# Kernel optimization log

Measured on AMD Instinct MI355X. Metric: run time of the kernel, lower is better.

Reference implementation:

```python
import jax, jax.numpy as jnp
import numpy as np

DIM = 1024
HEADS = 16
DIM_HEAD = 64
INNER = HEADS * DIM_HEAD
SCALE = DIM_HEAD ** -0.5


def setup_inputs() -> dict:
    key = jax.random.key(0)
    ks = jax.random.split(key, 9)
    B, N = 4, 4096
    x = jax.random.normal(ks[0], (B, N, DIM), dtype=jnp.float32)
    mask = jnp.ones((B, N), dtype=bool)
    s = 0.02
    W_qkv = jax.random.normal(ks[1], (DIM, INNER * 3), dtype=jnp.float32) * s
    w_q = jax.random.normal(ks[2], (DIM_HEAD,), dtype=jnp.float32) * s
    w_k = jax.random.normal(ks[3], (DIM_HEAD,), dtype=jnp.float32) * s
    W_r = jax.random.normal(ks[4], (DIM_HEAD, DIM_HEAD), dtype=jnp.float32) * s
    b_r = jnp.zeros((DIM_HEAD,), dtype=jnp.float32)
    W_out = jax.random.normal(ks[5], (INNER, DIM), dtype=jnp.float32) * s
    b_out = jnp.zeros((DIM,), dtype=jnp.float32)
    return {"x": x, "mask": mask, "W_qkv": W_qkv, "w_q": w_q, "w_k": w_k,
            "W_r": W_r, "b_r": b_r, "W_out": W_out, "b_out": b_out}


def reference(x, mask, W_qkv, w_q, w_k, W_r, b_r, W_out, b_out):
    B, N, D = x.shape
    h, dh = HEADS, DIM_HEAD
    mask_value = -jnp.finfo(x.dtype).max

    qkv = x @ W_qkv                                  # [B,N,3*inner]
    q, k, v = jnp.split(qkv, 3, axis=-1)
    tohead = lambda t: t.reshape(B, N, h, dh).transpose(0, 2, 1, 3)  # b h n d
    q, k, v = tohead(q), tohead(k), tohead(v)
    m = mask[:, None, :]                             # b 1 n

    # global query via softmax-pooled per-token logits
    q_logits = jnp.einsum('bhnd,d->bhn', q, w_q) * SCALE
    q_attn = jax.nn.softmax(jnp.where(m, q_logits, mask_value), axis=-1)
    global_q = jnp.einsum('bhn,bhnd->bhd', q_attn, q)[:, :, None, :]  # b h 1 d

    k = k * global_q
    k_logits = jnp.einsum('bhnd,d->bhn', k, w_k) * SCALE
    k_attn = jax.nn.softmax(jnp.where(m, k_logits, mask_value), axis=-1)
    global_k = jnp.einsum('bhn,bhnd->bhd', k_attn, k)[:, :, None, :]  # b h 1 d

    v = v * global_k
    r = jnp.einsum('bhnd,de->bhne', v, W_r) + b_r + q  # to_r(v) + q
    r = r.transpose(0, 2, 1, 3).reshape(B, N, h * dh)  # b n (h d)
    return r @ W_out + b_out
```

## Files before the change

### kernel.cpp

```cpp
#include <hip/hip_runtime.h>
#include <hip/hip_bf16.h>
#include <math.h>

#define B_    4
#define N_    4096
#define D_    1024
#define H_    16
#define DH_   64
#define M_TOT (B_ * N_)
#define QKV3  (3 * D_)
#define SCALE_ 0.125f
#define NSPLIT 4

typedef float f32x4 __attribute__((ext_vector_type(4)));
typedef __bf16 bf16x8 __attribute__((ext_vector_type(8)));
typedef unsigned short u16;
typedef unsigned int u32;

__device__ __forceinline__ float bf2f(u16 u) {
    union { u32 i; float f; } v; v.i = ((u32)u) << 16; return v.f;
}
__device__ __forceinline__ u16 f2bf(float f) {
    union { float f; u32 i; } v; v.f = f;
    u32 r = (v.i + 0x7fffu + ((v.i >> 16) & 1u)) >> 16;
    return (u16)r;
}

__global__ __launch_bounds__(256) void cvt_x(const float* __restrict__ in,
                                             u16* __restrict__ out, int n4) {
    int i = blockIdx.x * blockDim.x + threadIdx.x;
    if (i >= n4) return;
    float4 v = ((const float4*)in)[i];
    ushort4 o;
    o.x = f2bf(v.x); o.y = f2bf(v.y); o.z = f2bf(v.z); o.w = f2bf(v.w);
    ((ushort4*)out)[i] = o;
}

__global__ __launch_bounds__(256) void tcvt(const float* __restrict__ in,
                                            u16* __restrict__ out, int K, int N) {
    __shared__ float t[32][33];
    int n0 = blockIdx.x * 32, k0 = blockIdx.y * 32;
    int tx = threadIdx.x & 31, ty = threadIdx.x >> 5;
#pragma unroll
    for (int r = 0; r < 32; r += 8)
        t[ty + r][tx] = in[(size_t)(k0 + ty + r) * N + n0 + tx];
    __syncthreads();
#pragma unroll
    for (int r = 0; r < 32; r += 8)
        out[(size_t)(n0 + ty + r) * K + k0 + tx] = f2bf(t[tx][ty + r]);
}

#define BM 128
#define BN 128
#define BK 32

template <bool OUT_BF16, bool SCATTER>
__global__ __launch_bounds__(256) void gemm_bt(const u16* __restrict__ A,
                                               const u16* __restrict__ Bt,
                                               void* __restrict__ Cout,
                                               const float* __restrict__ bias,
                                               int M, int N, int K) {
    __shared__ u16 As[BM * BK];
    __shared__ u16 Bs[BN * BK];
    const int tid = threadIdx.x;
    const int wave = tid >> 6, lane = tid & 63;
    const int m0 = blockIdx.y * BM, n0 = blockIdx.x * BN;
    const int wr = wave & 1, wc = wave >> 1;

    f32x4 acc[4][4] = {};

    const int srow = lane >> 2;
    const int sk = (lane & 3) * 8;
    const u16* Ag = A + (size_t)(m0 + wave * 32 + srow) * K + sk;
    const u16* Bg = Bt + (size_t)(n0 + wave * 32 + srow) * K + sk;
    u16* Asw = &As[(wave * 32) * BK];
    u16* Bsw = &Bs[(wave * 32) * BK];

    const int fr = lane & 15;
    const int fk = (lane >> 4) * 8;

    for (int k0 = 0; k0 < K; k0 += BK) {
        __syncthreads();
        __builtin_amdgcn_global_load_lds(
            (__attribute__((address_space(1))) const void*)(Ag + k0),
            (__attribute__((address_space(3))) void*)Asw, 16, 0, 0);
        __builtin_amdgcn_global_load_lds(
            (__attribute__((address_space(1))) const void*)(Ag + k0 + 16 * K),
            (__attribute__((address_space(3))) void*)(Asw + 16 * BK), 16, 0, 0);
        __builtin_amdgcn_global_load_lds(
            (__attribute__((address_space(1))) const void*)(Bg + k0),
            (__attribute__((address_space(3))) void*)Bsw, 16, 0, 0);
        __builtin_amdgcn_global_load_lds(
            (__attribute__((address_space(1))) const void*)(Bg + k0 + 16 * K),
            (__attribute__((address_space(3))) void*)(Bsw + 16 * BK), 16, 0, 0);
        __syncthreads();

        bf16x8 af[4], bf[4];
#pragma unroll
        for (int i = 0; i < 4; i++)
            af[i] = *(const bf16x8*)&As[(wr * 64 + i * 16 + fr) * BK + fk];
#pragma unroll
        for (int i = 0; i < 4; i++)
            bf[i] = *(const bf16x8*)&Bs[(wc * 64 + i * 16 + fr) * BK + fk];
#pragma unroll
        for (int i = 0; i < 4; i++)
#pragma unroll
            for (int j = 0; j < 4; j++)
                acc[i][j] = __builtin_amdgcn_mfma_f32_16x16x32_bf16(af[i], bf[j], acc[i][j], 0, 0, 0);
    }

    const int cr = (lane >> 4) * 4;
    const int cc = lane & 15;
#pragma unroll
    for (int i = 0; i < 4; i++) {
#pragma unroll
        for (int j = 0; j < 4; j++) {
            const int row0 = m0 + wr * 64 + i * 16 + cr;
            const int col = n0 + wc * 64 + j * 16 + cc;
            const float bv = (!SCATTER && bias) ? bias[col] : 0.f;
#pragma unroll
            for (int r = 0; r < 4; r++) {
                const float v = acc[i][j][r] + bv;
                if (SCATTER) {
                    const int part = col >> 10, hh = (col >> 6) & (H_ - 1), e = col & (DH_ - 1);
                    const int row = row0 + r;
                    const int b = row >> 12, nn = row & (N_ - 1);
                    ((u16*)Cout)[(((size_t)(part * B_ + b) * H_ + hh) * N_ + nn) * DH_ + e] = f2bf(v);
                } else if (OUT_BF16) {
                    ((u16*)Cout)[(size_t)(row0 + r) * N + col] = f2bf(v);
                } else {
                    ((float*)Cout)[(size_t)(row0 + r) * N + col] = v;
                }
            }
        }
    }
}

template <bool KPHASE>
__global__ __launch_bounds__(256) void pool_partial(const u16* __restrict__ plane,
                                                    const float* __restrict__ wvec,
                                                    const float* __restrict__ gq_all,
                                                    float* __restrict__ part) {
    __shared__ float sm[32], sl[32], sacc[32][64];
    const int bh = blockIdx.x, s = blockIdx.y;
    const int tid = threadIdx.x;
    const int sub = tid >> 3, j = tid & 7;
    const size_t base = (size_t)bh * N_ * DH_ + (size_t)s * (N_ / NSPLIT) * DH_ + j * 8;

    float wv[8], gq[8];
#pragma unroll
    for (int i = 0; i < 8; i++) wv[i] = wvec[j * 8 + i];
    if (KPHASE) {
#pragma unroll
        for (int i = 0; i < 8; i++) gq[i] = gq_all[bh * 64 + j * 8 + i];
    }

    float m = -INFINITY, l = 0.f, acc[8];
#pragma unroll
    for (int i = 0; i < 8; i++) acc[i] = 0.f;
    for (int it = 0; it < N_ / NSPLIT / 32; it++) {
        const uint4 raw = *(const uint4*)(plane + base + (size_t)(it * 32 + sub) * DH_);
        const u16* pu = (const u16*)&raw;
        float f[8], p = 0.f;
#pragma unroll
        for (int i = 0; i < 8; i++) {
            f[i] = bf2f(pu[i]);
            if (KPHASE) f[i] *= gq[i];
            p += f[i] * wv[i];
        }
        p += __shfl_xor(p, 1); p += __shfl_xor(p, 2); p += __shfl_xor(p, 4);
        p *= SCALE_;
        const float mn = fmaxf(m, p);
        const float sc = __expf(m - mn);
        const float w = __expf(p - mn);
        m = mn; l = l * sc + w;
#pragma unroll
        for (int i = 0; i < 8; i++) acc[i] = acc[i] * sc + w * f[i];
    }
    if (j == 0) { sm[sub] = m; sl[sub] = l; }
#pragma unroll
    for (int i = 0; i < 8; i++) sacc[sub][j * 8 + i] = acc[i];
    __syncthreads();
    if (tid < 64) {
        float M = -INFINITY;
        for (int g = 0; g < 32; g++) M = fmaxf(M, sm[g]);
        float L = 0.f, ssum = 0.f;
        for (int g = 0; g < 32; g++) {
            const float e = __expf(sm[g] - M);
            L += sl[g] * e;
            ssum += sacc[g][tid] * e;
        }
        float* o = part + ((size_t)bh * NSPLIT + s) * 66;
        if (tid == 0) { o[0] = M; o[1] = L; }
        o[2 + tid] = ssum;
    }
}

__global__ __launch_bounds__(64) void pool_reduce(const float* __restrict__ part,
                                                  float* __restrict__ gout) {
    const int bh = blockIdx.x, e = threadIdx.x;
    float M = -INFINITY;
    for (int s = 0; s < NSPLIT; s++) M = fmaxf(M, part[((size_t)bh * NSPLIT + s) * 66]);
    float L = 0.f, ssum = 0.f;
    for (int s = 0; s < NSPLIT; s++) {
        const float* o = part + ((size_t)bh * NSPLIT + s) * 66;
        const float w = __expf(o[0] - M);
        L += o[1] * w;
        ssum += o[2 + e] * w;
    }
    gout[bh * 64 + e] = ssum / L;
}

__global__ __launch_bounds__(256) void apply_r_mfma(const u16* __restrict__ qkv,
                                                    const float* __restrict__ Wr,
                                                    const float* __restrict__ br,
                                                    const float* __restrict__ gk,
                                                    u16* __restrict__ rout) {
    __shared__ u16 Mt[64][136];
    const int bh = blockIdx.y;
    const int b = bh >> 4, h = bh & 15;
    const int tid = threadIdx.x, lane = tid & 63, wave = tid >> 6;

    for (int idx = tid; idx < 4096; idx += 256) {
        const int d = idx >> 6, e = idx & 63;
        Mt[e][d] = f2bf(gk[bh * 64 + d] * Wr[idx]);
        Mt[e][64 + d] = (d == e) ? (u16)0x3F80 : (u16)0;
    }
    __syncthreads();

    const size_t qbase = (size_t)bh * N_ * DH_;
    const size_t vbase = (size_t)(2 * B_ * H_ + bh) * N_ * DH_;
    const int row0 = blockIdx.x * 256 + wave * 64;
    const int fr = lane & 15;
    const int fk8 = (lane >> 4) * 8;
    f32x4 acc[4][4] = {};

#pragma unroll
    for (int ks = 0; ks < 4; ks++) {
        const int kd = ks * 32 + fk8;
        bf16x8 af[4], bf[4];
#pragma unroll
        for (int i = 0; i < 4; i++) {
            const int row = row0 + i * 16 + fr;
            const size_t off = (kd < 64) ? (vbase + (size_t)row * DH_ + kd)
                                         : (qbase + (size_t)row * DH_ + (kd - 64));
            af[i] = *(const bf16x8*)(qkv + off);
        }
#pragma unroll
        for (int j = 0; j < 4; j++)
            bf[j] = *(const bf16x8*)&Mt[j * 16 + fr][kd];
#pragma unroll
        for (int i = 0; i < 4; i++)
#pragma unroll
            for (int j = 0; j < 4; j++)
                acc[i][j] = __builtin_amdgcn_mfma_f32_16x16x32_bf16(af[i], bf[j], acc[i][j], 0, 0, 0);
    }

    const int cr = (lane >> 4) * 4;
    const int cc = lane & 15;
#pragma unroll
    for (int j = 0; j < 4; j++) {
        const int col = j * 16 + cc;
        const float bv = br[col];
#pragma unroll
        for (int i = 0; i < 4; i++) {
            const int row = row0 + i * 16 + cr;
#pragma unroll
            for (int r = 0; r < 4; r++)
                rout[(size_t)(b * N_ + row + r) * D_ + h * DH_ + col] = f2bf(acc[i][j][r] + bv);
        }
    }
}

extern "C" void kernel_launch(void* const* d_in, const int* in_sizes, int n_in,
                              void* d_out, int out_size, void* d_ws, size_t ws_size,
                              hipStream_t stream) {
    const float* x = (const float*)d_in[0];
    const float* W_qkv = (const float*)d_in[2];
    const float* w_q = (const float*)d_in[3];
    const float* w_k = (const float*)d_in[4];
    const float* W_r = (const float*)d_in[5];
    const float* b_r = (const float*)d_in[6];
    const float* W_out = (const float*)d_in[7];
    const float* b_out = (const float*)d_in[8];
    float* out = (float*)d_out;

    u16* xb = (u16*)d_ws;
    u16* wqkv = xb + (size_t)M_TOT * D_;
    u16* wout = wqkv + (size_t)QKV3 * D_;
    u16* qkv = wout + (size_t)D_ * D_;
    u16* rbuf = qkv + (size_t)M_TOT * QKV3;
    float* gq = (float*)(rbuf + (size_t)M_TOT * D_);
    float* gk = gq + 64 * 64;
    float* partb = gk + 64 * 64;

    cvt_x<<<(M_TOT * D_ / 4 + 255) / 256, 256, 0, stream>>>(x, xb, M_TOT * D_ / 4);
    tcvt<<<dim3(QKV3 / 32, D_ / 32), 256, 0, stream>>>(W_qkv, wqkv, D_, QKV3);
    tcvt<<<dim3(D_ / 32, D_ / 32), 256, 0, stream>>>(W_out, wout, D_, D_);

    gemm_bt<true, true><<<dim3(QKV3 / BN, M_TOT / BM), 256, 0, stream>>>(
        xb, wqkv, qkv, nullptr, M_TOT, QKV3, D_);

    pool_partial<false><<<dim3(64, NSPLIT), 256, 0, stream>>>(qkv, w_q, nullptr, partb);
    pool_reduce<<<64, 64, 0, stream>>>(partb, gq);
    pool_partial<true><<<dim3(64, NSPLIT), 256, 0, stream>>>(
        qkv + (size_t)(B_ * H_) * N_ * DH_, w_k, gq, partb);
    pool_reduce<<<64, 64, 0, stream>>>(partb, gk);

    apply_r_mfma<<<dim3(N_ / 256, 64), 256, 0, stream>>>(qkv, W_r, b_r, gk, rbuf);

    gemm_bt<false, false><<<dim3(D_ / BN, M_TOT / BM), 256, 0, stream>>>(
        rbuf, wout, out, b_out, M_TOT, D_, D_);
}
```

Baseline: 400.4 us.

## Fuse prep conversions into one kernel and fold pool reductions into consumers

Merges the x conversion and both weight transpose-conversions into a single prep launch. Removes the two pool_reduce kernels by having the K-phase pool kernel and apply_r_mfma each recompute the split-softmax merge into shared memory. Doubles NSPLIT so more blocks run the pooling passes, and adds one-ahead register prefetch in the pooling loop. Together these cut launch count and small serial kernels, at the cost of redundant reduction work in every consumer block.

New measurement: 387.1 us. -3.3%, faster.

```diff
diff --git a/kernel.cpp b/kernel.cpp
--- a/kernel.cpp
+++ b/kernel.cpp
@@ -10,7 +10,7 @@
 #define M_TOT (B_ * N_)
 #define QKV3  (3 * D_)
 #define SCALE_ 0.125f
-#define NSPLIT 4
+#define NSPLIT 8
 
 typedef float f32x4 __attribute__((ext_vector_type(4)));
 typedef __bf16 bf16x8 __attribute__((ext_vector_type(8)));
@@ -26,21 +26,29 @@
     return (u16)r;
 }
 
-__global__ __launch_bounds__(256) void cvt_x(const float* __restrict__ in,
-                                             u16* __restrict__ out, int n4) {
-    int i = blockIdx.x * blockDim.x + threadIdx.x;
-    if (i >= n4) return;
-    float4 v = ((const float4*)in)[i];
-    ushort4 o;
-    o.x = f2bf(v.x); o.y = f2bf(v.y); o.z = f2bf(v.z); o.w = f2bf(v.w);
-    ((ushort4*)out)[i] = o;
-}
-
-__global__ __launch_bounds__(256) void tcvt(const float* __restrict__ in,
-                                            u16* __restrict__ out, int K, int N) {
+__global__ __launch_bounds__(256) void prep(const float* __restrict__ x, u16* __restrict__ xb,
+                                            const float* __restrict__ Wqkv, u16* __restrict__ wqkv,
+                                            const float* __restrict__ Wout, u16* __restrict__ wout) {
     __shared__ float t[32][33];
-    int n0 = blockIdx.x * 32, k0 = blockIdx.y * 32;
-    int tx = threadIdx.x & 31, ty = threadIdx.x >> 5;
+    const int bid = blockIdx.x, tid = threadIdx.x;
+    if (bid < 16384) {
+        const int i = bid * 256 + tid;
+        float4 v = ((const float4*)x)[i];
+        ushort4 o;
+        o.x = f2bf(v.x); o.y = f2bf(v.y); o.z = f2bf(v.z); o.w = f2bf(v.w);
+        ((ushort4*)xb)[i] = o;
+        return;
+    }
+    const float* in; u16* out; int K, N, bx, by;
+    if (bid < 16384 + 3072) {
+        const int b2 = bid - 16384;
+        in = Wqkv; out = wqkv; K = D_; N = QKV3; bx = b2 % 96; by = b2 / 96;
+    } else {
+        const int b2 = bid - 19456;
+        in = Wout; out = wout; K = D_; N = D_; bx = b2 & 31; by = b2 >> 5;
+    }
+    const int n0 = bx * 32, k0 = by * 32;
+    const int tx = tid & 31, ty = tid >> 5;
 #pragma unroll
     for (int r = 0; r < 32; r += 8)
         t[ty + r][tx] = in[(size_t)(k0 + ty + r) * N + n0 + tx];
@@ -139,27 +147,48 @@
 template <bool KPHASE>
 __global__ __launch_bounds__(256) void pool_partial(const u16* __restrict__ plane,
                                                     const float* __restrict__ wvec,
-                                                    const float* __restrict__ gq_all,
+                                                    const float* __restrict__ partq,
                                                     float* __restrict__ part) {
     __shared__ float sm[32], sl[32], sacc[32][64];
+    __shared__ float gqsh[64];
     const int bh = blockIdx.x, s = blockIdx.y;
     const int tid = threadIdx.x;
     const int sub = tid >> 3, j = tid & 7;
     const size_t base = (size_t)bh * N_ * DH_ + (size_t)s * (N_ / NSPLIT) * DH_ + j * 8;
 
+    if (KPHASE) {
+        if (tid < 64) {
+            float M = -INFINITY;
+            for (int t = 0; t < NSPLIT; t++) M = fmaxf(M, partq[((size_t)bh * NSPLIT + t) * 66]);
+            float L = 0.f, ssum = 0.f;
+            for (int t = 0; t < NSPLIT; t++) {
+                const float* o = partq + ((size_t)bh * NSPLIT + t) * 66;
+                const float e = __expf(o[0] - M);
+                L += o[1] * e;
+                ssum += o[2 + tid] * e;
+            }
+            gqsh[tid] = ssum / L;
+        }
+        __syncthreads();
+    }
+
     float wv[8], gq[8];
 #pragma unroll
     for (int i = 0; i < 8; i++) wv[i] = wvec[j * 8 + i];
     if (KPHASE) {
 #pragma unroll
-        for (int i = 0; i < 8; i++) gq[i] = gq_all[bh * 64 + j * 8 + i];
+        for (int i = 0; i < 8; i++) gq[i] = gqsh[j * 8 + i];
     }
 
     float m = -INFINITY, l = 0.f, acc[8];
 #pragma unroll
     for (int i = 0; i < 8; i++) acc[i] = 0.f;
-    for (int it = 0; it < N_ / NSPLIT / 32; it++) {
-        const uint4 raw = *(const uint4*)(plane + base + (size_t)(it * 32 + sub) * DH_);
+    const int ITER = N_ / NSPLIT / 32;
+    uint4 raw = *(const uint4*)(plane + base + (size_t)sub * DH_);
+    for (int it = 0; it < ITER; it++) {
+        uint4 nxt;
+        if (it + 1 < ITER)
+            nxt = *(const uint4*)(plane + base + (size_t)((it + 1) * 32 + sub) * DH_);
         const u16* pu = (const u16*)&raw;
         float f[8], p = 0.f;
 #pragma unroll
@@ -176,6 +205,7 @@
         m = mn; l = l * sc + w;
 #pragma unroll
         for (int i = 0; i < 8; i++) acc[i] = acc[i] * sc + w * f[i];
+        raw = nxt;
     }
     if (j == 0) { sm[sub] = m; sl[sub] = l; }
 #pragma unroll
@@ -196,34 +226,34 @@
     }
 }
 
-__global__ __launch_bounds__(64) void pool_reduce(const float* __restrict__ part,
-                                                  float* __restrict__ gout) {
-    const int bh = blockIdx.x, e = threadIdx.x;
-    float M = -INFINITY;
-    for (int s = 0; s < NSPLIT; s++) M = fmaxf(M, part[((size_t)bh * NSPLIT + s) * 66]);
-    float L = 0.f, ssum = 0.f;
-    for (int s = 0; s < NSPLIT; s++) {
-        const float* o = part + ((size_t)bh * NSPLIT + s) * 66;
-        const float w = __expf(o[0] - M);
-        L += o[1] * w;
-        ssum += o[2 + e] * w;
-    }
-    gout[bh * 64 + e] = ssum / L;
-}
-
 __global__ __launch_bounds__(256) void apply_r_mfma(const u16* __restrict__ qkv,
                                                     const float* __restrict__ Wr,
                                                     const float* __restrict__ br,
-                                                    const float* __restrict__ gk,
+                                                    const float* __restrict__ partk,
                                                     u16* __restrict__ rout) {
     __shared__ u16 Mt[64][136];
+    __shared__ float gksh[64];
     const int bh = blockIdx.y;
     const int b = bh >> 4, h = bh & 15;
     const int tid = threadIdx.x, lane = tid & 63, wave = tid >> 6;
 
+    if (tid < 64) {
+        float M = -INFINITY;
+        for (int t = 0; t < NSPLIT; t++) M = fmaxf(M, partk[((size_t)bh * NSPLIT + t) * 66]);
+        float L = 0.f, ssum = 0.f;
+        for (int t = 0; t < NSPLIT; t++) {
+            const float* o = partk + ((size_t)bh * NSPLIT + t) * 66;
+            const float e = __expf(o[0] - M);
+            L += o[1] * e;
+            ssum += o[2 + tid] * e;
+        }
+        gksh[tid] = ssum / L;
+    }
+    __syncthreads();
+
     for (int idx = tid; idx < 4096; idx += 256) {
         const int d = idx >> 6, e = idx & 63;
-        Mt[e][d] = f2bf(gk[bh * 64 + d] * Wr[idx]);
+        Mt[e][d] = f2bf(gksh[d] * Wr[idx]);
         Mt[e][64 + d] = (d == e) ? (u16)0x3F80 : (u16)0;
     }
     __syncthreads();
@@ -290,24 +320,19 @@
     u16* wout = wqkv + (size_t)QKV3 * D_;
     u16* qkv = wout + (size_t)D_ * D_;
     u16* rbuf = qkv + (size_t)M_TOT * QKV3;
-    float* gq = (float*)(rbuf + (size_t)M_TOT * D_);
-    float* gk = gq + 64 * 64;
-    float* partb = gk + 64 * 64;
-
-    cvt_x<<<(M_TOT * D_ / 4 + 255) / 256, 256, 0, stream>>>(x, xb, M_TOT * D_ / 4);
-    tcvt<<<dim3(QKV3 / 32, D_ / 32), 256, 0, stream>>>(W_qkv, wqkv, D_, QKV3);
-    tcvt<<<dim3(D_ / 32, D_ / 32), 256, 0, stream>>>(W_out, wout, D_, D_);
+    float* partq = (float*)(rbuf + (size_t)M_TOT * D_);
+    float* partk = partq + 64 * NSPLIT * 66;
+
+    prep<<<16384 + 3072 + 1024, 256, 0, stream>>>(x, xb, W_qkv, wqkv, W_out, wout);
 
     gemm_bt<true, true><<<dim3(QKV3 / BN, M_TOT / BM), 256, 0, stream>>>(
         xb, wqkv, qkv, nullptr, M_TOT, QKV3, D_);
 
-    pool_partial<false><<<dim3(64, NSPLIT), 256, 0, stream>>>(qkv, w_q, nullptr, partb);
-    pool_reduce<<<64, 64, 0, stream>>>(partb, gq);
+    pool_partial<false><<<dim3(64, NSPLIT), 256, 0, stream>>>(qkv, w_q, nullptr, partq);
     pool_partial<true><<<dim3(64, NSPLIT), 256, 0, stream>>>(
-        qkv + (size_t)(B_ * H_) * N_ * DH_, w_k, gq, partb);
-    pool_reduce<<<64, 64, 0, stream>>>(partb, gk);
-
-    apply_r_mfma<<<dim3(N_ / 256, 64), 256, 0, stream>>>(qkv, W_r, b_r, gk, rbuf);
+        qkv + (size_t)(B_ * H_) * N_ * DH_, w_k, partq, partk);
+
+    apply_r_mfma<<<dim3(N_ / 256, 64), 256, 0, stream>>>(qkv, W_r, b_r, partk, rbuf);
 
     gemm_bt<false, false><<<dim3(D_ / BN, M_TOT / BM), 256, 0, stream>>>(
         rbuf, wout, out, b_out, M_TOT, D_, D_);
```
